# Kernel optimization log

Hardware: AMD Instinct MI355X
Metric: run time of the kernel (lower is better)

## Reference

```python
import jax, jax.numpy as jnp
import numpy as np

N = 20000      # nodes
E = 160000     # edges (avg degree 8)
DIM_IN = 6     # node_dim_in (3 pos + 3 extra)
DIM = 3        # spatial dim used for edge vectors
L = 128        # node_dim_latent
A = 8          # atom_type_embed_dim
NL = 4         # nlayers
NMAX = 20      # nmax_atom_types
MAX_R = 50.0   # max_radius
EIN = 2 * L + 2 * A + 1  # message MLP input: y_src, y_dst, edge_attr(2A+1)


def smooth_cutoff(x):
    # e3nn-style smooth cutoff: 1 for x<0.5, cos ramp on [0.5,1], 0 beyond
    u = 2.0 * (x - 1.0)
    y = 0.5 * (1.0 - jnp.cos(jnp.pi * u))
    y = jnp.where(u > 0.0, 0.0, y)
    y = jnp.where(u < -1.0, 1.0, y)
    return y


def setup_inputs() -> dict:
    key = jax.random.key(0)
    ks = jax.random.split(key, 14)
    x = jax.random.normal(ks[0], (N, DIM_IN), dtype=jnp.float32) * 2.0
    batch = jnp.zeros((N,), dtype=jnp.int32)  # single graph; unused (con_fnc=None)
    node_attr = jax.random.randint(ks[1], (N, 1), 0, NMAX, dtype=jnp.int32)
    edge_src = jax.random.randint(ks[2], (E,), 0, N, dtype=jnp.int32)
    off = jax.random.randint(ks[3], (E,), 1, N, dtype=jnp.int32)
    edge_dst = (edge_src + off) % N  # no self-loops -> edge_len > 0
    # orthogonal uplift/project weight (torch parametrizations.orthogonal)
    W, _ = jnp.linalg.qr(jax.random.normal(ks[4], (L, DIM_IN), dtype=jnp.float32))  # [L, DIM_IN], orthonormal cols
    embed = jax.random.normal(ks[5], (NMAX, A), dtype=jnp.float32)
    h = jnp.ones((NL,), dtype=jnp.float32) * 0.01
    msg_w1 = jax.random.normal(ks[6], (NL, EIN, L), dtype=jnp.float32) / np.sqrt(EIN)
    msg_b1 = jnp.zeros((NL, L), dtype=jnp.float32)
    msg_w2 = jax.random.normal(ks[7], (NL, L, L), dtype=jnp.float32) / np.sqrt(L)
    msg_b2 = jnp.zeros((NL, L), dtype=jnp.float32)
    node_w1 = jax.random.normal(ks[8], (NL, 2 * L, L), dtype=jnp.float32) / np.sqrt(2 * L)
    node_b1 = jnp.zeros((NL, L), dtype=jnp.float32)
    node_w2 = jax.random.normal(ks[9], (NL, L, L), dtype=jnp.float32) / np.sqrt(L)
    node_b2 = jnp.zeros((NL, L), dtype=jnp.float32)
    return {"x": x, "batch": batch, "node_attr": node_attr, "edge_src": edge_src,
            "edge_dst": edge_dst, "W": W, "embed": embed, "h": h,
            "msg_w1": msg_w1, "msg_b1": msg_b1, "msg_w2": msg_w2, "msg_b2": msg_b2,
            "node_w1": node_w1, "node_b1": node_b1, "node_w2": node_w2, "node_b2": node_b2}


def _block(y, edge_attr, edge_src, edge_dst, w1, b1, w2, b2, nw1, nb1, nw2, nb2):
    # gather-compute-scatter message passing block
    m_in = jnp.concatenate([y[edge_src], y[edge_dst], edge_attr], axis=-1)  # [E, EIN]
    m = jax.nn.silu(m_in @ w1 + b1) @ w2 + b2                                # [E, L]
    agg = jax.ops.segment_sum(m, edge_dst, num_segments=N)                   # [N, L]
    u = jnp.concatenate([y, agg], axis=-1)                                   # [N, 2L]
    return jax.nn.silu(u @ nw1 + nb1) @ nw2 + nb2                            # [N, L]


def reference(x, batch, node_attr, edge_src, edge_dst, W, embed, h,
              msg_w1, msg_b1, msg_w2, msg_b2, node_w1, node_b1, node_w2, node_b2):
    attr_e = embed[jnp.min(node_attr, axis=-1)]  # [N, A]
    y = x @ W.T                                   # uplift [N, L]
    y_old = y
    for i in range(NL):
        pos = x[:, :DIM]
        edge_vec = pos[edge_src] - pos[edge_dst]
        edge_len = jnp.linalg.norm(edge_vec, axis=1)
        w = smooth_cutoff(edge_len / MAX_R) / edge_len
        edge_attr = jnp.concatenate([attr_e[edge_src], attr_e[edge_dst], w[:, None]], axis=-1)
        y_new = _block(y, edge_attr, edge_src, edge_dst,
                       msg_w1[i], msg_b1[i], msg_w2[i], msg_b2[i],
                       node_w1[i], node_b1[i], node_w2[i], node_b2[i])
        # leapfrog (gamma = 0)
        tmp = y
        y = 2.0 * y - y_old - (h[i] ** 2) * y_new
        y_old = tmp
        x = y @ W  # project back to low dim
    cv = jnp.float32(-1.0)
    reg = jnp.float32(0.0)
    return (x, cv, cv, reg, reg)
```

## Files before the change

kernel.cpp:

```cpp
#include <hip/hip_runtime.h>
#include <hip/hip_bf16.h>
#include <math.h>

#define N_ 20000
#define NPAD_ 20032
#define E_ 160000
#define DIM_IN_ 6
#define L_ 128
#define A_ 8
#define NL_ 4
#define EIN_ 273
#define MAX_R_ 50.0f

typedef unsigned short u16;
typedef short bf16x8 __attribute__((ext_vector_type(8)));
typedef u16   u16x8  __attribute__((ext_vector_type(8)));
typedef float f32x4  __attribute__((ext_vector_type(4)));

static __device__ __forceinline__ float bf2f(u16 u) {
    return __uint_as_float(((unsigned)u) << 16);
}
static __device__ __forceinline__ u16 f2bf(float f) {
    unsigned b = __float_as_uint(f);
    return (u16)((b + 0x7FFF + ((b >> 16) & 1)) >> 16);
}
static __device__ __forceinline__ float silu(float v) {
    return v / (1.f + __expf(-v));
}


__global__ void k_init_y(const float* __restrict__ x, const float* __restrict__ W,
                         float* __restrict__ y, float* __restrict__ y_old) {
    int tid = blockIdx.x * blockDim.x + threadIdx.x;
    if (tid >= N_ * L_) return;
    int n = tid >> 7, l = tid & 127;
    float a = 0.f;
#pragma unroll
    for (int d = 0; d < DIM_IN_; ++d) a = fmaf(x[n * DIM_IN_ + d], W[l * DIM_IN_ + d], a);
    y[tid] = a;
    y_old[tid] = a;
}

__global__ void k_attr(const int* __restrict__ node_attr, const float* __restrict__ embed,
                       float* __restrict__ attr_e) {
    int tid = blockIdx.x * blockDim.x + threadIdx.x;
    if (tid >= N_ * A_) return;
    int n = tid >> 3, a = tid & 7;
    attr_e[tid] = embed[node_attr[n] * A_ + a];
}

__global__ void k_x(const float* __restrict__ y, const float* __restrict__ W,
                    float* __restrict__ x_out) {
    int tid = blockIdx.x * blockDim.x + threadIdx.x;
    if (tid >= N_ * DIM_IN_) return;
    int n = tid / DIM_IN_, d = tid % DIM_IN_;
    float a = 0.f;
    for (int l = 0; l < L_; ++l) a = fmaf(y[(size_t)n * L_ + l], W[l * DIM_IN_ + d], a);
    x_out[tid] = a;
}

__global__ void k_edge_w(const float* __restrict__ xp, const int* __restrict__ esrc,
                         const int* __restrict__ edst, const int* __restrict__ perm,
                         float* __restrict__ w_csr) {
    int e = blockIdx.x * blockDim.x + threadIdx.x;
    if (e >= E_) return;
    int s = esrc[e], d = edst[e];
    float dx = xp[s * DIM_IN_ + 0] - xp[d * DIM_IN_ + 0];
    float dy = xp[s * DIM_IN_ + 1] - xp[d * DIM_IN_ + 1];
    float dz = xp[s * DIM_IN_ + 2] - xp[d * DIM_IN_ + 2];
    float len = sqrtf(dx * dx + dy * dy + dz * dz);
    float u = 2.f * (len / MAX_R_ - 1.f);
    float cv;
    if (u > 0.f)       cv = 0.f;
    else if (u < -1.f) cv = 1.f;
    else               cv = 0.5f * (1.f - cosf(3.14159265358979323846f * u));
    w_csr[perm[e]] = cv / len;
}

__global__ void k_scalars(float* __restrict__ tail) {
    int j = threadIdx.x;
    if (j < 4) tail[j] = (j < 2) ? -1.0f : 0.0f;
}


__global__ void k_hist(const int* __restrict__ edst, int* __restrict__ deg) {
    int e = blockIdx.x * blockDim.x + threadIdx.x;
    if (e < E_) atomicAdd(&deg[edst[e]], 1);
}

#define SCAN_CH 20
__global__ __launch_bounds__(1024) void k_scan(const int* __restrict__ deg,
                                               int* __restrict__ rowptr,
                                               int* __restrict__ cursor) {
    __shared__ int s[1024];
    int t = threadIdx.x;
    int base = t * SCAN_CH;
    int local[SCAN_CH];
    int sum = 0;
#pragma unroll
    for (int j = 0; j < SCAN_CH; ++j) {
        int n = base + j;
        int d = (n < N_) ? deg[n] : 0;
        local[j] = d; sum += d;
    }
    s[t] = sum;
    __syncthreads();
    for (int off = 1; off < 1024; off <<= 1) {
        int v = (t >= off) ? s[t - off] : 0;
        __syncthreads();
        s[t] += v;
        __syncthreads();
    }
    int run = t ? s[t - 1] : 0;
#pragma unroll
    for (int j = 0; j < SCAN_CH; ++j) {
        int n = base + j;
        if (n < N_) { rowptr[n] = run; cursor[n] = run; run += local[j]; }
    }
    if (t == 1023) rowptr[N_] = run;
}

__global__ void k_fill(const int* __restrict__ esrc, const int* __restrict__ edst,
                       int* __restrict__ cursor, int* __restrict__ perm,
                       int* __restrict__ csr_src) {
    int e = blockIdx.x * blockDim.x + threadIdx.x;
    if (e >= E_) return;
    int p = atomicAdd(&cursor[edst[e]], 1);
    perm[e] = p;
    csr_src[p] = esrc[e];
}

__global__ void k_prep(const float* __restrict__ mw1, const float* __restrict__ mb1,
                       const float* __restrict__ nw1, const float* __restrict__ nw2,
                       u16* __restrict__ w1cat_t, u16* __restrict__ nw1at,
                       u16* __restrict__ nw2t,
                       float* __restrict__ w1attr, float* __restrict__ bcat,
                       float* __restrict__ wr272) {
    int idx = blockIdx.x * 256 + threadIdx.x;
    if (idx < NL_ * 256 * 128) {
        int i = idx >> 15; int rem = idx & 32767; int cc = rem >> 7; int k = rem & 127;
        int row = (cc < 128) ? k : 128 + k;
        w1cat_t[idx] = f2bf(mw1[(size_t)i * EIN_ * L_ + row * L_ + (cc & 127)]);
        return;
    }
    idx -= NL_ * 256 * 128;
    if (idx < NL_ * 128 * 128) {
        int i = idx >> 14; int rem = idx & 16383; int c = rem >> 7; int k = rem & 127;
        nw1at[idx] = f2bf(nw1[(size_t)i * 2 * L_ * L_ + k * L_ + c]);
        return;
    }
    idx -= NL_ * 128 * 128;
    if (idx < NL_ * 128 * 128) {
        int i = idx >> 14; int rem = idx & 16383; int c = rem >> 7; int k = rem & 127;
        nw2t[idx] = f2bf(nw2[(size_t)i * L_ * L_ + k * L_ + c]);
        return;
    }
    idx -= NL_ * 128 * 128;
    if (idx < NL_ * 8 * 256) {
        int i = idx >> 11; int rem = idx & 2047; int j = rem >> 8; int cc = rem & 255;
        int row = (cc < 128) ? 256 + j : 264 + j;
        w1attr[idx] = mw1[(size_t)i * EIN_ * L_ + row * L_ + (cc & 127)];
        return;
    }
    idx -= NL_ * 8 * 256;
    if (idx < NL_ * 256) {
        int i = idx >> 8; int cc = idx & 255;
        bcat[idx] = (cc < 128) ? 0.f : mb1[i * L_ + cc - 128];
        return;
    }
    idx -= NL_ * 256;
    if (idx < NL_ * 128) {
        int i = idx >> 7; int c = idx & 127;
        wr272[idx] = mw1[(size_t)i * EIN_ * L_ + 272 * L_ + c];
    }
}
#define PREP_TOTAL (NL_*256*128 + 2*NL_*128*128 + NL_*8*256 + NL_*256 + NL_*128)

__global__ void k_prep2(const float* __restrict__ mw2, const float* __restrict__ mb2,
                        const float* __restrict__ nw1,
                        u16* __restrict__ W2nt, float* __restrict__ bvec) {
    int idx = blockIdx.x * 256 + threadIdx.x;
    if (idx < NL_ * 128 * 128) {
        int i = idx >> 14; int rem = idx & 16383; int c = rem >> 7; int k = rem & 127;
        const float* w2row = &mw2[(size_t)i * L_ * L_ + k * L_];
        const float* nb    = &nw1[(size_t)i * 2 * L_ * L_ + 128 * L_ + c];
        float a = 0.f;
        for (int j = 0; j < 128; ++j) a = fmaf(w2row[j], nb[(size_t)j * L_], a);
        W2nt[idx] = f2bf(a);
        return;
    }
    idx -= NL_ * 128 * 128;
    if (idx < NL_ * 128) {
        int i = idx >> 7; int c = idx & 127;
        const float* b2 = &mb2[i * L_];
        const float* nb = &nw1[(size_t)i * 2 * L_ * L_ + 128 * L_ + c];
        float a = 0.f;
        for (int j = 0; j < 128; ++j) a = fmaf(b2[j], nb[(size_t)j * L_], a);
        bvec[idx] = a;
    }
}
#define PREP2_TOTAL (NL_*128*128 + NL_*128)

__global__ __launch_bounds__(256) void k_pre(
    const float* __restrict__ y, const float* __restrict__ attr_e,
    const u16* __restrict__ w1cat_t,
    const float* __restrict__ w1attr,
    const float* __restrict__ bcat,
    u16* __restrict__ P) {
    __shared__ u16   s_a[64 * 136];
    __shared__ float s_attr[64 * 8];
    __shared__ float s_w1a[8 * 128];
    __shared__ float s_bc[128];

    const int t  = threadIdx.x;
    const int n0 = blockIdx.x * 64;
    const int cb = blockIdx.y;

    for (int i = t; i < 64 * 16; i += 256) {
        int r = i >> 4, ch = i & 15;
        int n = n0 + r;
        u16x8 v;
        if (n < N_) {
            const float4* p = (const float4*)&y[(size_t)n * L_ + ch * 8];
            float4 f0 = p[0], f1 = p[1];
            v[0] = f2bf(f0.x); v[1] = f2bf(f0.y); v[2] = f2bf(f0.z); v[3] = f2bf(f0.w);
            v[4] = f2bf(f1.x); v[5] = f2bf(f1.y); v[6] = f2bf(f1.z); v[7] = f2bf(f1.w);
        } else {
#pragma unroll
            for (int j = 0; j < 8; ++j) v[j] = 0;
        }
        *(u16x8*)&s_a[r * 136 + ch * 8] = v;
    }
    for (int i = t; i < 64 * 2; i += 256) {
        int r = i >> 1, half = i & 1;
        int n = n0 + r;
        float4 v = make_float4(0.f, 0.f, 0.f, 0.f);
        if (n < N_) v = *(const float4*)&attr_e[(size_t)n * A_ + half * 4];
        *(float4*)&s_attr[r * 8 + half * 4] = v;
    }
    for (int i = t; i < 8 * 128; i += 256) {
        int j = i >> 7, c = i & 127;
        s_w1a[i] = w1attr[j * 256 + cb * 128 + c];
    }
    if (t < 128) s_bc[t] = bcat[cb * 128 + t];
    __syncthreads();

    const int l  = t & 63, w = t >> 6;
    const int r0 = w * 16;
    const int lr = l & 15, lk = l >> 4;

    bf16x8 a[4];
#pragma unroll
    for (int ks = 0; ks < 4; ++ks)
        a[ks] = *(const bf16x8*)&s_a[(r0 + lr) * 136 + ks * 32 + lk * 8];

#pragma unroll
    for (int ct = 0; ct < 8; ++ct) {
        int c = ct * 16 + lr;
        float bb = s_bc[c];
        f32x4 acc = {bb, bb, bb, bb};
#pragma unroll
        for (int ks = 0; ks < 4; ++ks) {
            bf16x8 b = *(const bf16x8*)&w1cat_t[(size_t)(cb * 128 + c) * 128 + ks * 32 + lk * 8];
            acc = __builtin_amdgcn_mfma_f32_16x16x32_bf16(a[ks], b, acc, 0, 0, 0);
        }
#pragma unroll
        for (int i = 0; i < 4; ++i) {
            int r = r0 + lk * 4 + i;
            int n = n0 + r;
            if (n < N_) {
                float v = acc[i];
#pragma unroll
                for (int j = 0; j < 8; ++j) v = fmaf(s_attr[r * 8 + j], s_w1a[j * 128 + c], v);
                P[(size_t)n * 256 + cb * 128 + c] = f2bf(v);
            }
        }
    }
}

__global__ __launch_bounds__(256) void k_agg(
    const u16* __restrict__ P, const float* __restrict__ w_csr,
    const int* __restrict__ csr_src, const int* __restrict__ rowptr,
    const float* __restrict__ wr272,
    u16* __restrict__ Hsum) {
    const int t = threadIdx.x;
    const int node = blockIdx.x * 4 + (t >> 6);
    const int l = t & 63;

    const int beg = rowptr[node], end = rowptr[node + 1];
    const float wr0 = wr272[2 * l], wr1 = wr272[2 * l + 1];
    unsigned pdu = *(const unsigned*)&P[(size_t)node * 256 + 128 + 2 * l];
    const float pd0 = bf2f((u16)pdu), pd1 = bf2f((u16)(pdu >> 16));

    float h0 = 0.f, h1 = 0.f;
    for (int i = beg; i < end; ++i) {
        int s = csr_src[i];
        float w = w_csr[i];
        unsigned psu = *(const unsigned*)&P[(size_t)s * 256 + 2 * l];
        float v0 = bf2f((u16)psu)         + pd0 + w * wr0;
        float v1 = bf2f((u16)(psu >> 16)) + pd1 + w * wr1;
        h0 += silu(v0);
        h1 += silu(v1);
    }
    unsigned out = (unsigned)f2bf(h0) | ((unsigned)f2bf(h1) << 16);
    *(unsigned*)&Hsum[(size_t)node * 128 + 2 * l] = out;
}

__global__ __launch_bounds__(256) void k_node(
    float* __restrict__ y, float* __restrict__ y_old,
    const u16* __restrict__ Hsum, const int* __restrict__ rowptr,
    const u16* __restrict__ nw1at,
    const u16* __restrict__ W2nt,
    const u16* __restrict__ nw2t,
    const float* __restrict__ bvec,
    const float* __restrict__ nb1,
    const float* __restrict__ nb2,
    const float* __restrict__ hvec, int layer) {
    __shared__ u16   s_a[64 * 136];
    __shared__ u16   s_h[64 * 136];
    __shared__ float s_deg[64];
    __shared__ float s_bv[128], s_b1[128], s_b2v[128];

    const int t  = threadIdx.x;
    const int n0 = blockIdx.x * 64;

    for (int i = t; i < 64 * 16; i += 256) {
        int r = i >> 4, ch = i & 15;
        int n = n0 + r;
        u16x8 v;
        if (n < N_) {
            const float4* p = (const float4*)&y[(size_t)n * L_ + ch * 8];
            float4 f0 = p[0], f1 = p[1];
            v[0] = f2bf(f0.x); v[1] = f2bf(f0.y); v[2] = f2bf(f0.z); v[3] = f2bf(f0.w);
            v[4] = f2bf(f1.x); v[5] = f2bf(f1.y); v[6] = f2bf(f1.z); v[7] = f2bf(f1.w);
        } else {
#pragma unroll
            for (int j = 0; j < 8; ++j) v[j] = 0;
        }
        *(u16x8*)&s_a[r * 136 + ch * 8] = v;
    }
    if (t < 128) { s_bv[t] = bvec[t]; s_b1[t] = nb1[t]; s_b2v[t] = nb2[t]; }
    else if (t < 192) {
        int r = t - 128, n = n0 + r;
        s_deg[r] = (n < N_) ? (float)(rowptr[n + 1] - rowptr[n]) : 0.f;
    }
    __syncthreads();

    const int l  = t & 63, w = t >> 6;
    const int r0 = w * 16;
    const int lr = l & 15, lk = l >> 4;

    bf16x8 ay[4], ah[4];
    const int nfr = n0 + r0 + lr;
#pragma unroll
    for (int ks = 0; ks < 4; ++ks) {
        ay[ks] = *(const bf16x8*)&s_a[(r0 + lr) * 136 + ks * 32 + lk * 8];
        ah[ks] = *(const bf16x8*)&Hsum[(size_t)nfr * 128 + ks * 32 + lk * 8];
    }

#pragma unroll
    for (int ct = 0; ct < 8; ++ct) {
        int c = ct * 16 + lr;
        f32x4 acc;
#pragma unroll
        for (int i = 0; i < 4; ++i)
            acc[i] = s_b1[c] + s_deg[r0 + lk * 4 + i] * s_bv[c];
#pragma unroll
        for (int ks = 0; ks < 4; ++ks) {
            bf16x8 b1f = *(const bf16x8*)&nw1at[(size_t)c * 128 + ks * 32 + lk * 8];
            acc = __builtin_amdgcn_mfma_f32_16x16x32_bf16(ay[ks], b1f, acc, 0, 0, 0);
        }
#pragma unroll
        for (int ks = 0; ks < 4; ++ks) {
            bf16x8 b2f = *(const bf16x8*)&W2nt[(size_t)c * 128 + ks * 32 + lk * 8];
            acc = __builtin_amdgcn_mfma_f32_16x16x32_bf16(ah[ks], b2f, acc, 0, 0, 0);
        }
#pragma unroll
        for (int i = 0; i < 4; ++i)
            s_h[(r0 + lk * 4 + i) * 136 + c] = f2bf(silu(acc[i]));
    }
    __syncthreads();

    bf16x8 a2[4];
#pragma unroll
    for (int ks = 0; ks < 4; ++ks)
        a2[ks] = *(const bf16x8*)&s_h[(r0 + lr) * 136 + ks * 32 + lk * 8];

    float hh = hvec[layer];
    float h2 = hh * hh;

#pragma unroll
    for (int ct = 0; ct < 8; ++ct) {
        int c = ct * 16 + lr;
        float bb = s_b2v[c];
        f32x4 acc = {bb, bb, bb, bb};
#pragma unroll
        for (int ks = 0; ks < 4; ++ks) {
            bf16x8 b = *(const bf16x8*)&nw2t[(size_t)c * 128 + ks * 32 + lk * 8];
            acc = __builtin_amdgcn_mfma_f32_16x16x32_bf16(a2[ks], b, acc, 0, 0, 0);
        }
#pragma unroll
        for (int i = 0; i < 4; ++i) {
            int n = n0 + r0 + lk * 4 + i;
            if (n < N_) {
                size_t idx = (size_t)n * L_ + c;
                float yv = y[idx], yo = y_old[idx];
                y_old[idx] = yv;
                y[idx] = 2.f * yv - yo - h2 * acc[i];
            }
        }
    }
}


#define ALLOC(ptr, T, count) T* ptr = (T*)base; base += (((size_t)(count) * sizeof(T)) + 255) / 256 * 256;

extern "C" void kernel_launch(void* const* d_in, const int* in_sizes, int n_in,
                              void* d_out, int out_size, void* d_ws, size_t ws_size,
                              hipStream_t stream) {
    const float* x_in      = (const float*)d_in[0];
    const int*   node_attr = (const int*)  d_in[2];
    const int*   esrc      = (const int*)  d_in[3];
    const int*   edst      = (const int*)  d_in[4];
    const float* W         = (const float*)d_in[5];
    const float* embed     = (const float*)d_in[6];
    const float* hvec      = (const float*)d_in[7];
    const float* mw1       = (const float*)d_in[8];
    const float* mb1       = (const float*)d_in[9];
    const float* mw2       = (const float*)d_in[10];
    const float* mb2       = (const float*)d_in[11];
    const float* nw1       = (const float*)d_in[12];
    const float* nb1       = (const float*)d_in[13];
    const float* nw2       = (const float*)d_in[14];
    const float* nb2       = (const float*)d_in[15];
    float* out = (float*)d_out;

    char* base = (char*)d_ws;
    ALLOC(y,       float, (size_t)N_ * L_);
    ALLOC(y_old,   float, (size_t)N_ * L_);
    ALLOC(x_cur,   float, (size_t)N_ * DIM_IN_);
    ALLOC(attr_e,  float, (size_t)N_ * A_);
    ALLOC(P,       u16,   (size_t)N_ * 256);
    ALLOC(Hsum,    u16,   (size_t)NPAD_ * 128);
    ALLOC(w_csr,   float, E_);
    ALLOC(csr_src, int,   E_);
    ALLOC(perm,    int,   E_);
    ALLOC(deg,     int,   N_);
    ALLOC(rowptr,  int,   N_ + 1);
    ALLOC(cursor,  int,   N_);
    ALLOC(w1cat_t, u16,   (size_t)NL_ * 256 * 128);
    ALLOC(nw1at,   u16,   (size_t)NL_ * 128 * 128);
    ALLOC(nw2t,    u16,   (size_t)NL_ * 128 * 128);
    ALLOC(W2nt,    u16,   (size_t)NL_ * 128 * 128);
    ALLOC(w1attr,  float, (size_t)NL_ * 8 * 256);
    ALLOC(bcat,    float, (size_t)NL_ * 256);
    ALLOC(wr272,   float, (size_t)NL_ * 128);
    ALLOC(bvec,    float, (size_t)NL_ * 128);

    hipMemsetAsync(deg, 0, (size_t)N_ * sizeof(int), stream);
    k_prep<<<(PREP_TOTAL + 255) / 256, 256, 0, stream>>>(
        mw1, mb1, nw1, nw2, w1cat_t, nw1at, nw2t, w1attr, bcat, wr272);
    k_prep2<<<(PREP2_TOTAL + 255) / 256, 256, 0, stream>>>(mw2, mb2, nw1, W2nt, bvec);
    k_init_y<<<(N_ * L_ + 255) / 256, 256, 0, stream>>>(x_in, W, y, y_old);
    k_attr<<<(N_ * A_ + 255) / 256, 256, 0, stream>>>(node_attr, embed, attr_e);
    k_hist<<<(E_ + 255) / 256, 256, 0, stream>>>(edst, deg);
    k_scan<<<1, 1024, 0, stream>>>(deg, rowptr, cursor);
    k_fill<<<(E_ + 255) / 256, 256, 0, stream>>>(esrc, edst, cursor, perm, csr_src);

    for (int i = 0; i < NL_; ++i) {
        const float* xp = (i == 0) ? x_in : x_cur;
        if (i > 0)
            k_x<<<(N_ * DIM_IN_ + 255) / 256, 256, 0, stream>>>(y, W, x_cur);
        k_edge_w<<<(E_ + 255) / 256, 256, 0, stream>>>(xp, esrc, edst, perm, w_csr);
        k_pre<<<dim3(313, 2), 256, 0, stream>>>(
            y, attr_e,
            w1cat_t + (size_t)i * 256 * 128,
            w1attr + (size_t)i * 8 * 256,
            bcat + (size_t)i * 256,
            P);
        k_agg<<<N_ / 4, 256, 0, stream>>>(
            P, w_csr, csr_src, rowptr,
            wr272 + (size_t)i * 128,
            Hsum);
        k_node<<<313, 256, 0, stream>>>(
            y, y_old, Hsum, rowptr,
            nw1at + (size_t)i * 128 * 128,
            W2nt + (size_t)i * 128 * 128,
            nw2t + (size_t)i * 128 * 128,
            bvec + (size_t)i * 128,
            nb1 + (size_t)i * L_,
            nb2 + (size_t)i * L_,
            hvec, i);
    }

    k_x<<<(N_ * DIM_IN_ + 255) / 256, 256, 0, stream>>>(y, W, out);
    k_scalars<<<1, 4, 0, stream>>>(out + (size_t)N_ * DIM_IN_);
}
```

Measured before the change: 522.5 us.

## Fuse edge-weight computation into aggregation and merge k_pre column blocks

```diff
diff --git a/kernel.cpp b/kernel.cpp
--- a/kernel.cpp
+++ b/kernel.cpp
@@ -49,6 +49,22 @@
     attr_e[tid] = embed[node_attr[n] * A_ + a];
 }
 
+__global__ void k_pos(const float* __restrict__ y, const float* __restrict__ W,
+                      const float* __restrict__ x_in, int layer,
+                      float* __restrict__ pos4) {
+    int tid = blockIdx.x * blockDim.x + threadIdx.x;
+    if (tid >= N_ * 4) return;
+    int n = tid >> 2, d = tid & 3;
+    float v = 0.f;
+    if (d < 3) {
+        if (layer == 0) v = x_in[n * DIM_IN_ + d];
+        else {
+            for (int l = 0; l < L_; ++l) v = fmaf(y[(size_t)n * L_ + l], W[l * DIM_IN_ + d], v);
+        }
+    }
+    pos4[tid] = v;
+}
+
 __global__ void k_x(const float* __restrict__ y, const float* __restrict__ W,
                     float* __restrict__ x_out) {
     int tid = blockIdx.x * blockDim.x + threadIdx.x;
@@ -57,24 +73,6 @@
     float a = 0.f;
     for (int l = 0; l < L_; ++l) a = fmaf(y[(size_t)n * L_ + l], W[l * DIM_IN_ + d], a);
     x_out[tid] = a;
-}
-
-__global__ void k_edge_w(const float* __restrict__ xp, const int* __restrict__ esrc,
-                         const int* __restrict__ edst, const int* __restrict__ perm,
-                         float* __restrict__ w_csr) {
-    int e = blockIdx.x * blockDim.x + threadIdx.x;
-    if (e >= E_) return;
-    int s = esrc[e], d = edst[e];
-    float dx = xp[s * DIM_IN_ + 0] - xp[d * DIM_IN_ + 0];
-    float dy = xp[s * DIM_IN_ + 1] - xp[d * DIM_IN_ + 1];
-    float dz = xp[s * DIM_IN_ + 2] - xp[d * DIM_IN_ + 2];
-    float len = sqrtf(dx * dx + dy * dy + dz * dz);
-    float u = 2.f * (len / MAX_R_ - 1.f);
-    float cv;
-    if (u > 0.f)       cv = 0.f;
-    else if (u < -1.f) cv = 1.f;
-    else               cv = 0.5f * (1.f - cosf(3.14159265358979323846f * u));
-    w_csr[perm[e]] = cv / len;
 }
 
 __global__ void k_scalars(float* __restrict__ tail) {
@@ -121,12 +119,10 @@
 }
 
 __global__ void k_fill(const int* __restrict__ esrc, const int* __restrict__ edst,
-                       int* __restrict__ cursor, int* __restrict__ perm,
-                       int* __restrict__ csr_src) {
+                       int* __restrict__ cursor, int* __restrict__ csr_src) {
     int e = blockIdx.x * blockDim.x + threadIdx.x;
     if (e >= E_) return;
     int p = atomicAdd(&cursor[edst[e]], 1);
-    perm[e] = p;
     csr_src[p] = esrc[e];
 }
 
@@ -209,12 +205,11 @@
     u16* __restrict__ P) {
     __shared__ u16   s_a[64 * 136];
     __shared__ float s_attr[64 * 8];
-    __shared__ float s_w1a[8 * 128];
-    __shared__ float s_bc[128];
+    __shared__ float s_w1a[8 * 256];
+    __shared__ float s_bc[256];
 
     const int t  = threadIdx.x;
     const int n0 = blockIdx.x * 64;
-    const int cb = blockIdx.y;
 
     for (int i = t; i < 64 * 16; i += 256) {
         int r = i >> 4, ch = i & 15;
@@ -238,11 +233,8 @@
         if (n < N_) v = *(const float4*)&attr_e[(size_t)n * A_ + half * 4];
         *(float4*)&s_attr[r * 8 + half * 4] = v;
     }
-    for (int i = t; i < 8 * 128; i += 256) {
-        int j = i >> 7, c = i & 127;
-        s_w1a[i] = w1attr[j * 256 + cb * 128 + c];
-    }
-    if (t < 128) s_bc[t] = bcat[cb * 128 + t];
+    for (int i = t; i < 8 * 256; i += 256) s_w1a[i] = w1attr[i];
+    if (t < 256) s_bc[t] = bcat[t];
     __syncthreads();
 
     const int l  = t & 63, w = t >> 6;
@@ -255,31 +247,34 @@
         a[ks] = *(const bf16x8*)&s_a[(r0 + lr) * 136 + ks * 32 + lk * 8];
 
 #pragma unroll
-    for (int ct = 0; ct < 8; ++ct) {
-        int c = ct * 16 + lr;
-        float bb = s_bc[c];
-        f32x4 acc = {bb, bb, bb, bb};
-#pragma unroll
-        for (int ks = 0; ks < 4; ++ks) {
-            bf16x8 b = *(const bf16x8*)&w1cat_t[(size_t)(cb * 128 + c) * 128 + ks * 32 + lk * 8];
-            acc = __builtin_amdgcn_mfma_f32_16x16x32_bf16(a[ks], b, acc, 0, 0, 0);
-        }
-#pragma unroll
-        for (int i = 0; i < 4; ++i) {
-            int r = r0 + lk * 4 + i;
-            int n = n0 + r;
-            if (n < N_) {
-                float v = acc[i];
-#pragma unroll
-                for (int j = 0; j < 8; ++j) v = fmaf(s_attr[r * 8 + j], s_w1a[j * 128 + c], v);
-                P[(size_t)n * 256 + cb * 128 + c] = f2bf(v);
+    for (int cb = 0; cb < 2; ++cb) {
+#pragma unroll
+        for (int ct = 0; ct < 8; ++ct) {
+            int cc = cb * 128 + ct * 16 + lr;
+            float bb = s_bc[cc];
+            f32x4 acc = {bb, bb, bb, bb};
+#pragma unroll
+            for (int ks = 0; ks < 4; ++ks) {
+                bf16x8 b = *(const bf16x8*)&w1cat_t[(size_t)cc * 128 + ks * 32 + lk * 8];
+                acc = __builtin_amdgcn_mfma_f32_16x16x32_bf16(a[ks], b, acc, 0, 0, 0);
             }
+#pragma unroll
+            for (int i = 0; i < 4; ++i) {
+                int r = r0 + lk * 4 + i;
+                int n = n0 + r;
+                if (n < N_) {
+                    float v = acc[i];
+#pragma unroll
+                    for (int j = 0; j < 8; ++j) v = fmaf(s_attr[r * 8 + j], s_w1a[j * 256 + cc], v);
+                    P[(size_t)n * 256 + cc] = f2bf(v);
+                }
+            }
         }
     }
 }
 
 __global__ __launch_bounds__(256) void k_agg(
-    const u16* __restrict__ P, const float* __restrict__ w_csr,
+    const u16* __restrict__ P, const float* __restrict__ pos4,
     const int* __restrict__ csr_src, const int* __restrict__ rowptr,
     const float* __restrict__ wr272,
     u16* __restrict__ Hsum) {
@@ -291,16 +286,34 @@
     const float wr0 = wr272[2 * l], wr1 = wr272[2 * l + 1];
     unsigned pdu = *(const unsigned*)&P[(size_t)node * 256 + 128 + 2 * l];
     const float pd0 = bf2f((u16)pdu), pd1 = bf2f((u16)(pdu >> 16));
+    const float4 pn = *(const float4*)&pos4[node * 4];
 
     float h0 = 0.f, h1 = 0.f;
-    for (int i = beg; i < end; ++i) {
-        int s = csr_src[i];
-        float w = w_csr[i];
-        unsigned psu = *(const unsigned*)&P[(size_t)s * 256 + 2 * l];
-        float v0 = bf2f((u16)psu)         + pd0 + w * wr0;
-        float v1 = bf2f((u16)(psu >> 16)) + pd1 + w * wr1;
-        h0 += silu(v0);
-        h1 += silu(v1);
+    for (int cbeg = beg; cbeg < end; cbeg += 64) {
+        const int cnt = min(64, end - cbeg);
+        int   srcl = 0;
+        float wl   = 0.f;
+        if (l < cnt) {
+            srcl = csr_src[cbeg + l];
+            float4 ps = *(const float4*)&pos4[srcl * 4];
+            float dx = ps.x - pn.x, dy = ps.y - pn.y, dz = ps.z - pn.z;
+            float len = sqrtf(dx * dx + dy * dy + dz * dz);
+            float u = 2.f * (len / MAX_R_ - 1.f);
+            float cv;
+            if (u > 0.f)       cv = 0.f;
+            else if (u < -1.f) cv = 1.f;
+            else               cv = 0.5f * (1.f - cosf(3.14159265358979323846f * u));
+            wl = cv / len;
+        }
+        for (int i = 0; i < cnt; ++i) {
+            int   s = __shfl(srcl, i, 64);
+            float w = __shfl(wl,   i, 64);
+            unsigned psu = *(const unsigned*)&P[(size_t)s * 256 + 2 * l];
+            float v0 = bf2f((u16)psu)         + pd0 + w * wr0;
+            float v1 = bf2f((u16)(psu >> 16)) + pd1 + w * wr1;
+            h0 += silu(v0);
+            h1 += silu(v1);
+        }
     }
     unsigned out = (unsigned)f2bf(h0) | ((unsigned)f2bf(h1) << 16);
     *(unsigned*)&Hsum[(size_t)node * 128 + 2 * l] = out;
@@ -438,13 +451,11 @@
     char* base = (char*)d_ws;
     ALLOC(y,       float, (size_t)N_ * L_);
     ALLOC(y_old,   float, (size_t)N_ * L_);
-    ALLOC(x_cur,   float, (size_t)N_ * DIM_IN_);
     ALLOC(attr_e,  float, (size_t)N_ * A_);
+    ALLOC(pos4,    float, (size_t)N_ * 4);
     ALLOC(P,       u16,   (size_t)N_ * 256);
     ALLOC(Hsum,    u16,   (size_t)NPAD_ * 128);
-    ALLOC(w_csr,   float, E_);
     ALLOC(csr_src, int,   E_);
-    ALLOC(perm,    int,   E_);
     ALLOC(deg,     int,   N_);
     ALLOC(rowptr,  int,   N_ + 1);
     ALLOC(cursor,  int,   N_);
@@ -465,21 +476,18 @@
     k_attr<<<(N_ * A_ + 255) / 256, 256, 0, stream>>>(node_attr, embed, attr_e);
     k_hist<<<(E_ + 255) / 256, 256, 0, stream>>>(edst, deg);
     k_scan<<<1, 1024, 0, stream>>>(deg, rowptr, cursor);
-    k_fill<<<(E_ + 255) / 256, 256, 0, stream>>>(esrc, edst, cursor, perm, csr_src);
+    k_fill<<<(E_ + 255) / 256, 256, 0, stream>>>(esrc, edst, cursor, csr_src);
 
     for (int i = 0; i < NL_; ++i) {
-        const float* xp = (i == 0) ? x_in : x_cur;
-        if (i > 0)
-            k_x<<<(N_ * DIM_IN_ + 255) / 256, 256, 0, stream>>>(y, W, x_cur);
-        k_edge_w<<<(E_ + 255) / 256, 256, 0, stream>>>(xp, esrc, edst, perm, w_csr);
-        k_pre<<<dim3(313, 2), 256, 0, stream>>>(
+        k_pos<<<(N_ * 4 + 255) / 256, 256, 0, stream>>>(y, W, x_in, i, pos4);
+        k_pre<<<313, 256, 0, stream>>>(
             y, attr_e,
             w1cat_t + (size_t)i * 256 * 128,
             w1attr + (size_t)i * 8 * 256,
             bcat + (size_t)i * 256,
             P);
         k_agg<<<N_ / 4, 256, 0, stream>>>(
-            P, w_csr, csr_src, rowptr,
+            P, pos4, csr_src, rowptr,
             wr272 + (size_t)i * 128,
             Hsum);
         k_node<<<313, 256, 0, stream>>>(
```

Measured after the change: 495.8 us. -5.1%, faster.
